# Kernel optimization log

Hardware: AMD Instinct MI355X
Metric: run time of the kernel (lower is better)

The kernel has to match this reference:

```python
import jax, jax.numpy as jnp
import numpy as np
import math

D_MODEL = 1024
N_HEADS = 16
D_K = D_MODEL // N_HEADS
B, S = 4, 2048
NEG_INF = -1e9


def setup_inputs() -> dict:
    key = jax.random.key(0)
    ks = jax.random.split(key, 12)
    scale = 1.0 / math.sqrt(D_MODEL)
    inp = {
        "q": jax.random.normal(ks[0], (B, S, D_MODEL), jnp.float32),
        "k": jax.random.normal(ks[1], (B, S, D_MODEL), jnp.float32),
        "v": jax.random.normal(ks[2], (B, S, D_MODEL), jnp.float32),
        "mask": jax.random.randint(ks[3], (1, 1, S, S), 0, 2, jnp.int32),
        "w_q": jax.random.normal(ks[4], (D_MODEL, D_MODEL), jnp.float32) * scale,
        "b_q": jnp.zeros((D_MODEL,), jnp.float32),
        "w_k": jax.random.normal(ks[5], (D_MODEL, D_MODEL), jnp.float32) * scale,
        "b_k": jnp.zeros((D_MODEL,), jnp.float32),
        "w_v": jax.random.normal(ks[6], (D_MODEL, D_MODEL), jnp.float32) * scale,
        "b_v": jnp.zeros((D_MODEL,), jnp.float32),
        "w_o": jax.random.normal(ks[7], (D_MODEL, D_MODEL), jnp.float32) * scale,
        "b_o": jnp.zeros((D_MODEL,), jnp.float32),
    }
    return inp


def reference(q, k, v, mask, w_q, b_q, w_k, b_k, w_v, b_v, w_o, b_o):
    # Linear projections (torch Linear: x @ W.T + b)
    query = q @ w_q.T + b_q
    key_p = k @ w_k.T + b_k
    value = v @ w_v.T + b_v
    # [B,S,D] -> [B,H,S,d_k]
    def split_heads(x):
        return x.reshape(B, S, N_HEADS, D_K).transpose(0, 2, 1, 3)
    qh, kh, vh = split_heads(query), split_heads(key_p), split_heads(value)
    # scores: [B,H,S,S]
    scores = jnp.einsum('bhqd,bhkd->bhqk', qh, kh) / math.sqrt(D_K)
    scores = jnp.where(mask == 0, NEG_INF, scores)
    probs = jax.nn.softmax(scores, axis=-1)
    # attention output: [B,H,S,d_k] -> [B,S,D]
    x = jnp.einsum('bhqk,bhkd->bhqd', probs, vh)
    x = x.transpose(0, 2, 1, 3).reshape(B, S, D_MODEL)
    return x @ w_o.T + b_o
```

## Files before the change

### kernel.cpp

```cpp
#include <hip/hip_runtime.h>


typedef __bf16  bf16x8 __attribute__((ext_vector_type(8)));
typedef float   f32x4  __attribute__((ext_vector_type(4)));
typedef float   f32x16 __attribute__((ext_vector_type(16)));
typedef float   fv4    __attribute__((ext_vector_type(4)));
typedef unsigned int uint;
typedef __attribute__((address_space(3))) char        as3c;
typedef __attribute__((address_space(1))) const char  as1c;

static __device__ __forceinline__ void gload16(const void* g, void* l) {
  __builtin_amdgcn_global_load_lds((as1c*)g, (as3c*)l, 16, 0, 0);
}
static __device__ __forceinline__ f32x4 mfma16(bf16x8 a, bf16x8 b, f32x4 c) {
  return __builtin_amdgcn_mfma_f32_16x16x32_bf16(a, b, c, 0, 0, 0);
}
static __device__ __forceinline__ f32x16 mfma32(bf16x8 a, bf16x8 b, f32x16 c) {
  return __builtin_amdgcn_mfma_f32_32x32x16_bf16(a, b, c, 0, 0, 0);
}
static __device__ __forceinline__ void st4bf(void* dst, float a, float b, float c, float d) {
  union { __bf16 h[4]; unsigned long long u; } x;
  x.h[0] = (__bf16)a; x.h[1] = (__bf16)b; x.h[2] = (__bf16)c; x.h[3] = (__bf16)d;
  *(unsigned long long*)dst = x.u;
}
static __device__ __forceinline__ uint pk2(float lo, float hi) {
  union { __bf16 h[2]; uint u; } x;
  x.h[0] = (__bf16)lo; x.h[1] = (__bf16)hi; return x.u;
}
static __device__ __forceinline__ f32x16 fconst16(float c) {
  f32x16 z;
#pragma unroll
  for (int i = 0; i < 16; ++i) z[i] = c;
  return z;
}

__global__ void cvt_w(const float* __restrict__ w0, const float* __restrict__ w1,
                      const float* __restrict__ w2, const float* __restrict__ w3,
                      __bf16* __restrict__ dst) {
  int i = (blockIdx.x * 256 + threadIdx.x) * 4;
  int seg = i >> 20, off = i & 1048575;
  const float* s = seg == 0 ? w0 : seg == 1 ? w1 : seg == 2 ? w2 : w3;
  fv4 v = *(const fv4*)(s + off);
  st4bf(dst + i, v[0], v[1], v[2], v[3]);
}

__global__ void pack_mask(const int* __restrict__ mask,
                          unsigned long long* __restrict__ out) {
  int wid = threadIdx.x >> 6, lane = threadIdx.x & 63;
  for (int w = blockIdx.x * 4 + wid; w < 2048 * 32; w += gridDim.x * 4) {
    int v = mask[(w >> 5) * 2048 + (w & 31) * 64 + lane];
    unsigned long long bits = __ballot(v != 0);
    if (lane == 0) out[w] = bits;
  }
}

template<int MODE>
__global__ __launch_bounds__(256, 3)
void gemm_bt(const void* __restrict__ Ap, const __bf16* __restrict__ Bw,
             const float* __restrict__ bias, void* __restrict__ Cp) {
  __shared__ __align__(16) char lds_a[2][8192];
  __shared__ __align__(16) char lds_b[2][8192];
  const int t = threadIdx.x;
  const int lane = t & 63, lr = lane & 15, lg = lane >> 4;
  const int wid = t >> 6, wr = wid >> 1, wc = wid & 1;
  const int bid = blockIdx.x;
  const int xcd = bid & 7, local = bid >> 3;
  const int rowStart = (xcd * 8 + (local >> 3)) * 128;
  const int colStart = (local & 7) * 128;

  const float*  Af = (const float*)Ap;
  const __bf16* Ah = (const __bf16*)Ap;
  fv4 ra[4];

  auto loadA = [&](int kt) {
    if constexpr (MODE < 3) {
#pragma unroll
      for (int rr = 0; rr < 4; ++rr) {
        int lin = rr * 1024 + t * 4;
        int row = lin >> 5, col = lin & 31;
        ra[rr] = *(const fv4*)(Af + (rowStart + row) * 1024 + kt + col);
      }
    }
  };
  auto writeA = [&](int buf) {
    if constexpr (MODE < 3) {
#pragma unroll
      for (int rr = 0; rr < 4; ++rr) {
        int lin = rr * 1024 + t * 4;
        st4bf(&lds_a[buf][lin * 2], ra[rr][0], ra[rr][1], ra[rr][2], ra[rr][3]);
      }
    }
  };
  auto stageB = [&](int buf, int kt) {
    if constexpr (MODE == 3) {
#pragma unroll
      for (int rr = 0; rr < 2; ++rr) {
        int lin = rr * 2048 + t * 8;
        int row = lin >> 5, col = lin & 31;
        gload16(Ah + (rowStart + row) * 1024 + kt + col, &lds_a[buf][lin * 2]);
      }
    }
#pragma unroll
    for (int rr = 0; rr < 2; ++rr) {
      int lin = rr * 2048 + t * 8;
      int row = lin >> 5, col = lin & 31;
      gload16(Bw + (colStart + row) * 1024 + kt + col, &lds_b[buf][lin * 2]);
    }
  };

  f32x4 acc[4][4];
#pragma unroll
  for (int m = 0; m < 4; ++m)
#pragma unroll
    for (int n = 0; n < 4; ++n) {
      acc[m][n][0] = 0.f; acc[m][n][1] = 0.f; acc[m][n][2] = 0.f; acc[m][n][3] = 0.f;
    }

  loadA(0); stageB(0, 0);
  int cur = 0;
  for (int it = 0; it < 32; ++it) {
    writeA(cur);
    __syncthreads();
    if (it + 1 < 32) { loadA((it + 1) * 32); stageB(cur ^ 1, (it + 1) * 32); }

    bf16x8 af[4], bfr[4];
#pragma unroll
    for (int m = 0; m < 4; ++m)
      af[m] = *(const bf16x8*)(&lds_a[cur][(wr * 64 + m * 16 + lr) * 64 + lg * 16]);
#pragma unroll
    for (int n = 0; n < 4; ++n)
      bfr[n] = *(const bf16x8*)(&lds_b[cur][(wc * 64 + n * 16 + lr) * 64 + lg * 16]);
#pragma unroll
    for (int m = 0; m < 4; ++m)
#pragma unroll
      for (int n = 0; n < 4; ++n)
        acc[m][n] = mfma16(af[m], bfr[n], acc[m][n]);
    cur ^= 1;
  }

#pragma unroll
  for (int n = 0; n < 4; ++n) {
    int col = colStart + wc * 64 + n * 16 + lr;
    float bv = bias[col];
#pragma unroll
    for (int m = 0; m < 4; ++m) {
      int rowb = rowStart + wr * 64 + m * 16 + lg * 4;
      if constexpr (MODE == 0 || MODE == 1) {
        __bf16* C = (__bf16*)Cp;
#pragma unroll
        for (int r = 0; r < 4; ++r) {
          float val = acc[m][n][r] + bv;
          if constexpr (MODE == 0) val *= 0.18033688011112042f;
          C[(rowb + r) * 1024 + col] = (__bf16)val;
        }
      } else if constexpr (MODE == 2) {
        __bf16* C = (__bf16*)Cp;
        int bb = rowb >> 11, s = rowb & 2047;
        st4bf(C + ((bb << 10) + col) * 2048 + s,
              acc[m][n][0] + bv, acc[m][n][1] + bv,
              acc[m][n][2] + bv, acc[m][n][3] + bv);
      } else {
        float* C = (float*)Cp;
#pragma unroll
        for (int r = 0; r < 4; ++r)
          C[(rowb + r) * 1024 + col] = acc[m][n][r] + bv;
      }
    }
  }
}

__global__ __launch_bounds__(256, 3)
void attn_fwd(const __bf16* __restrict__ Qp, const __bf16* __restrict__ Kp,
              const __bf16* __restrict__ Vt, const unsigned long long* __restrict__ Mb,
              __bf16* __restrict__ Xb) {
  __shared__ __align__(16) char lds[2][16384];
  const int t = threadIdx.x;
  const int lane = t & 63;
  const int l31 = lane & 31, hi = lane >> 5;
  const int wid = t >> 6;
  const int bid = blockIdx.x;
  const int nid = (bid & 7) * 128 + (bid >> 3);
  const int qblk = nid & 15, bh = nid >> 4;
  const int b = bh >> 4, h = bh & 15;
  const int q = qblk * 128 + wid * 32 + l31;

  bf16x8 qf[4];
#pragma unroll
  for (int c = 0; c < 4; ++c)
    qf[c] = *(const bf16x8*)(Qp + (b * 2048 + q) * 1024 + h * 64 + c * 16 + hi * 8);

  f32x16 xacc0 = fconst16(0.f), xacc1 = fconst16(0.f);
  float l_r = 0.f;

  auto stage = [&](int buf, int k0) {
#pragma unroll
    for (int rr = 0; rr < 2; ++rr) {
      int o = rr * 4096 + t * 16;
      int row = o >> 7, cb = o & 127;
      int cbs = cb ^ ((row & 7) << 4);
      gload16(Kp + (b * 2048 + k0 + row) * 1024 + h * 64 + (cbs >> 1), &lds[buf][o]);
      gload16(Vt + (bh * 64 + row) * 2048 + k0 + (cbs >> 1), &lds[buf][8192 + o]);
    }
  };

  stage(0, 0);
  int cur = 0;
  for (int it = 0; it < 32; ++it) {
    __syncthreads();
    if (it + 1 < 32) stage(cur ^ 1, (it + 1) * 64);

    const char* lk = lds[cur];
    const char* lv = lds[cur] + 8192;

    f32x16 sc0 = fconst16(-16.f), sc1 = fconst16(-16.f);
#pragma unroll
    for (int c = 0; c < 4; ++c) {
      {
        int krow = l31;
        int byo = (c * 32 + hi * 16) ^ ((krow & 7) << 4);
        bf16x8 kf = *(const bf16x8*)(lk + krow * 128 + byo);
        sc0 = mfma32(kf, qf[c], sc0);
      }
      {
        int krow = 32 + l31;
        int byo = (c * 32 + hi * 16) ^ ((krow & 7) << 4);
        bf16x8 kf = *(const bf16x8*)(lk + krow * 128 + byo);
        sc1 = mfma32(kf, qf[c], sc1);
      }
    }
    asm volatile("" : "+v"(sc0), "+v"(sc1));

    unsigned long long mw = Mb[q * 32 + it];
    uint mm0 = ((uint)mw) >> (4 * hi);
    uint mm1 = ((uint)(mw >> 32)) >> (4 * hi);
    float rs = 0.f;
#pragma unroll
    for (int r = 0; r < 16; ++r) {
      const int bit = (r & 3) + 8 * (r >> 2);
      float p0 = __builtin_amdgcn_exp2f(sc0[r]);
      float p1 = __builtin_amdgcn_exp2f(sc1[r]);
      uint z0 = (uint)((int)(mm0 << (31 - bit)) >> 31);
      uint z1 = (uint)((int)(mm1 << (31 - bit)) >> 31);
      p0 = __uint_as_float(__float_as_uint(p0) & z0);
      p1 = __uint_as_float(__float_as_uint(p1) & z1);
      sc0[r] = p0; sc1[r] = p1;
      rs += p0 + p1;
    }
    rs += __shfl_xor(rs, 32);
    l_r += rs;

    uint cp0[8], cp1[8];
#pragma unroll
    for (int m = 0; m < 8; ++m) {
      cp0[m] = pk2(sc0[2 * m], sc0[2 * m + 1]);
      cp1[m] = pk2(sc1[2 * m], sc1[2 * m + 1]);
    }

#define PV_SLICE(CPK, S) do {                                               \
      uint w0 = CPK[4 * ((S) & 1) + 0], w2 = CPK[4 * ((S) & 1) + 2];        \
      uint w1 = CPK[4 * ((S) & 1) + 1], w3 = CPK[4 * ((S) & 1) + 3];        \
      asm volatile("v_permlane32_swap_b32 %0, %1" : "+v"(w0), "+v"(w2));    \
      asm volatile("v_permlane32_swap_b32 %0, %1" : "+v"(w1), "+v"(w3));    \
      union { uint u[4]; bf16x8 v8; } pu;                                   \
      pu.u[0] = w0; pu.u[1] = w1; pu.u[2] = w2; pu.u[3] = w3;               \
      { int vrow = l31;                                                     \
        int byo = (((S) * 32 + hi * 16)) ^ ((vrow & 7) << 4);               \
        bf16x8 vf = *(const bf16x8*)(lv + vrow * 128 + byo);                \
        xacc0 = mfma32(vf, pu.v8, xacc0); }                                 \
      { int vrow = 32 + l31;                                                \
        int byo = (((S) * 32 + hi * 16)) ^ ((vrow & 7) << 4);               \
        bf16x8 vf = *(const bf16x8*)(lv + vrow * 128 + byo);                \
        xacc1 = mfma32(vf, pu.v8, xacc1); }                                 \
    } while (0)
    PV_SLICE(cp0, 0); PV_SLICE(cp0, 1); PV_SLICE(cp1, 2); PV_SLICE(cp1, 3);
#undef PV_SLICE
    cur ^= 1;
  }

  float inv = 1.f / l_r;
  __bf16* orow = Xb + (b * 2048 + q) * 1024 + h * 64 + 4 * hi;
#pragma unroll
  for (int g = 0; g < 4; ++g) {
    st4bf(orow + 8 * g,      xacc0[4 * g] * inv, xacc0[4 * g + 1] * inv,
                             xacc0[4 * g + 2] * inv, xacc0[4 * g + 3] * inv);
    st4bf(orow + 32 + 8 * g, xacc1[4 * g] * inv, xacc1[4 * g + 1] * inv,
                             xacc1[4 * g + 2] * inv, xacc1[4 * g + 3] * inv);
  }
}

extern "C" void kernel_launch(void* const* d_in, const int* in_sizes, int n_in,
                              void* d_out, int out_size, void* d_ws, size_t ws_size,
                              hipStream_t stream) {
  const float* q    = (const float*)d_in[0];
  const float* k    = (const float*)d_in[1];
  const float* v    = (const float*)d_in[2];
  const int*   mask = (const int*)d_in[3];
  const float* wq   = (const float*)d_in[4];
  const float* bq   = (const float*)d_in[5];
  const float* wk   = (const float*)d_in[6];
  const float* bk   = (const float*)d_in[7];
  const float* wv   = (const float*)d_in[8];
  const float* bv   = (const float*)d_in[9];
  const float* wo   = (const float*)d_in[10];
  const float* bo   = (const float*)d_in[11];

  char* ws = (char*)d_ws;
  __bf16* Wb  = (__bf16*)(ws);
  __bf16* Qp  = (__bf16*)(ws + (size_t)(8u  << 20));
  __bf16* Kp  = (__bf16*)(ws + (size_t)(24u << 20));
  __bf16* Vtb = (__bf16*)(ws + (size_t)(40u << 20));
  __bf16* Xb  = (__bf16*)(ws + (size_t)(56u << 20));
  unsigned long long* Mb = (unsigned long long*)(ws + (size_t)(72u << 20));

  cvt_w<<<4096, 256, 0, stream>>>(wq, wk, wv, wo, Wb);
  pack_mask<<<1024, 256, 0, stream>>>(mask, Mb);
  gemm_bt<0><<<512, 256, 0, stream>>>(q, Wb,              bq, Qp);
  gemm_bt<1><<<512, 256, 0, stream>>>(k, Wb + (1u << 20), bk, Kp);
  gemm_bt<2><<<512, 256, 0, stream>>>(v, Wb + (2u << 20), bv, Vtb);
  attn_fwd<<<1024, 256, 0, stream>>>(Qp, Kp, Vtb, Mb, Xb);
  gemm_bt<3><<<512, 256, 0, stream>>>(Xb, Wb + (3u << 20), bo, (float*)d_out);
}
```

Measured before the change: 419.0 us.

## Merge prep and QKV launches, compute softmax row sum via MFMA, add setprio

```diff
diff --git a/kernel.cpp b/kernel.cpp
--- a/kernel.cpp
+++ b/kernel.cpp
@@ -34,30 +34,132 @@
   return z;
 }
 
-__global__ void cvt_w(const float* __restrict__ w0, const float* __restrict__ w1,
-                      const float* __restrict__ w2, const float* __restrict__ w3,
-                      __bf16* __restrict__ dst) {
-  int i = (blockIdx.x * 256 + threadIdx.x) * 4;
-  int seg = i >> 20, off = i & 1048575;
-  const float* s = seg == 0 ? w0 : seg == 1 ? w1 : seg == 2 ? w2 : w3;
-  fv4 v = *(const fv4*)(s + off);
-  st4bf(dst + i, v[0], v[1], v[2], v[3]);
-}
-
-__global__ void pack_mask(const int* __restrict__ mask,
-                          unsigned long long* __restrict__ out) {
-  int wid = threadIdx.x >> 6, lane = threadIdx.x & 63;
-  for (int w = blockIdx.x * 4 + wid; w < 2048 * 32; w += gridDim.x * 4) {
-    int v = mask[(w >> 5) * 2048 + (w & 31) * 64 + lane];
-    unsigned long long bits = __ballot(v != 0);
-    if (lane == 0) out[w] = bits;
-  }
-}
-
-template<int MODE>
+__global__ void prep(const float* __restrict__ w0, const float* __restrict__ w1,
+                     const float* __restrict__ w2, const float* __restrict__ w3,
+                     __bf16* __restrict__ dst,
+                     const int* __restrict__ mask,
+                     unsigned long long* __restrict__ out) {
+  int bid = blockIdx.x;
+  if (bid < 4096) {
+    int i = (bid * 256 + threadIdx.x) * 4;
+    int seg = i >> 20, off = i & 1048575;
+    const float* s = seg == 0 ? w0 : seg == 1 ? w1 : seg == 2 ? w2 : w3;
+    fv4 v = *(const fv4*)(s + off);
+    st4bf(dst + i, v[0], v[1], v[2], v[3]);
+  } else {
+    int pb = bid - 4096;
+    int wid = threadIdx.x >> 6, lane = threadIdx.x & 63;
+    for (int w = pb * 4 + wid; w < 2048 * 32; w += 1024 * 4) {
+      int v = mask[(w >> 5) * 2048 + (w & 31) * 64 + lane];
+      unsigned long long bits = __ballot(v != 0);
+      if (lane == 0) out[w] = bits;
+    }
+  }
+}
+
 __global__ __launch_bounds__(256, 3)
-void gemm_bt(const void* __restrict__ Ap, const __bf16* __restrict__ Bw,
-             const float* __restrict__ bias, void* __restrict__ Cp) {
+void qkv_proj(const float* __restrict__ qin, const float* __restrict__ kin,
+              const float* __restrict__ vin, const __bf16* __restrict__ Wb,
+              const float* __restrict__ bq, const float* __restrict__ bk,
+              const float* __restrict__ bv,
+              __bf16* __restrict__ Qp, __bf16* __restrict__ Kp,
+              __bf16* __restrict__ Vt) {
+  __shared__ __align__(16) char lds_a[2][8192];
+  __shared__ __align__(16) char lds_b[2][8192];
+  const int t = threadIdx.x;
+  const int lane = t & 63, lr = lane & 15, lg = lane >> 4;
+  const int wid = t >> 6, wr = wid >> 1, wc = wid & 1;
+  const int x = blockIdx.x;
+  const int which = x >> 9, inner = x & 511;
+  const int xcd = inner & 7, local = inner >> 3;
+  const int rowStart = (xcd * 8 + (local >> 3)) * 128;
+  const int colStart = (local & 7) * 128;
+
+  const float*  A    = which == 0 ? qin : which == 1 ? kin : vin;
+  const __bf16* W    = Wb + (which << 20);
+  const float*  bias = which == 0 ? bq : which == 1 ? bk : bv;
+
+  fv4 ra[4];
+  auto loadA = [&](int kt) {
+#pragma unroll
+    for (int rr = 0; rr < 4; ++rr) {
+      int lin = rr * 1024 + t * 4;
+      int row = lin >> 5, col = lin & 31;
+      ra[rr] = *(const fv4*)(A + (rowStart + row) * 1024 + kt + col);
+    }
+  };
+  auto writeA = [&](int buf) {
+#pragma unroll
+    for (int rr = 0; rr < 4; ++rr) {
+      int lin = rr * 1024 + t * 4;
+      st4bf(&lds_a[buf][lin * 2], ra[rr][0], ra[rr][1], ra[rr][2], ra[rr][3]);
+    }
+  };
+  auto stageB = [&](int buf, int kt) {
+#pragma unroll
+    for (int rr = 0; rr < 2; ++rr) {
+      int lin = rr * 2048 + t * 8;
+      int row = lin >> 5, col = lin & 31;
+      gload16(W + (colStart + row) * 1024 + kt + col, &lds_b[buf][lin * 2]);
+    }
+  };
+
+  f32x4 acc[4][4];
+#pragma unroll
+  for (int m = 0; m < 4; ++m)
+#pragma unroll
+    for (int n = 0; n < 4; ++n) {
+      acc[m][n][0] = 0.f; acc[m][n][1] = 0.f; acc[m][n][2] = 0.f; acc[m][n][3] = 0.f;
+    }
+
+  loadA(0); stageB(0, 0);
+  int cur = 0;
+  for (int it = 0; it < 32; ++it) {
+    writeA(cur);
+    __syncthreads();
+    if (it + 1 < 32) { loadA((it + 1) * 32); stageB(cur ^ 1, (it + 1) * 32); }
+
+    bf16x8 af[4], bfr[4];
+#pragma unroll
+    for (int m = 0; m < 4; ++m)
+      af[m] = *(const bf16x8*)(&lds_a[cur][(wr * 64 + m * 16 + lr) * 64 + lg * 16]);
+#pragma unroll
+    for (int n = 0; n < 4; ++n)
+      bfr[n] = *(const bf16x8*)(&lds_b[cur][(wc * 64 + n * 16 + lr) * 64 + lg * 16]);
+#pragma unroll
+    for (int m = 0; m < 4; ++m)
+#pragma unroll
+      for (int n = 0; n < 4; ++n)
+        acc[m][n] = mfma16(af[m], bfr[n], acc[m][n]);
+    cur ^= 1;
+  }
+
+  const float scale = which == 0 ? 0.18033688011112042f : 1.0f;
+#pragma unroll
+  for (int n = 0; n < 4; ++n) {
+    int col = colStart + wc * 64 + n * 16 + lr;
+    float bvv = bias[col];
+#pragma unroll
+    for (int m = 0; m < 4; ++m) {
+      int rowb = rowStart + wr * 64 + m * 16 + lg * 4;
+      if (which == 2) {
+        int bb = rowb >> 11, s = rowb & 2047;
+        st4bf(Vt + ((bb << 10) + col) * 2048 + s,
+              acc[m][n][0] + bvv, acc[m][n][1] + bvv,
+              acc[m][n][2] + bvv, acc[m][n][3] + bvv);
+      } else {
+        __bf16* C = which == 0 ? Qp : Kp;
+#pragma unroll
+        for (int r = 0; r < 4; ++r)
+          C[(rowb + r) * 1024 + col] = (__bf16)((acc[m][n][r] + bvv) * scale);
+      }
+    }
+  }
+}
+
+__global__ __launch_bounds__(256, 3)
+void gemm_out(const __bf16* __restrict__ Ah, const __bf16* __restrict__ Bw,
+              const float* __restrict__ bias, float* __restrict__ Cp) {
   __shared__ __align__(16) char lds_a[2][8192];
   __shared__ __align__(16) char lds_b[2][8192];
   const int t = threadIdx.x;
@@ -68,42 +170,12 @@
   const int rowStart = (xcd * 8 + (local >> 3)) * 128;
   const int colStart = (local & 7) * 128;
 
-  const float*  Af = (const float*)Ap;
-  const __bf16* Ah = (const __bf16*)Ap;
-  fv4 ra[4];
-
-  auto loadA = [&](int kt) {
-    if constexpr (MODE < 3) {
-#pragma unroll
-      for (int rr = 0; rr < 4; ++rr) {
-        int lin = rr * 1024 + t * 4;
-        int row = lin >> 5, col = lin & 31;
-        ra[rr] = *(const fv4*)(Af + (rowStart + row) * 1024 + kt + col);
-      }
-    }
-  };
-  auto writeA = [&](int buf) {
-    if constexpr (MODE < 3) {
-#pragma unroll
-      for (int rr = 0; rr < 4; ++rr) {
-        int lin = rr * 1024 + t * 4;
-        st4bf(&lds_a[buf][lin * 2], ra[rr][0], ra[rr][1], ra[rr][2], ra[rr][3]);
-      }
-    }
-  };
-  auto stageB = [&](int buf, int kt) {
-    if constexpr (MODE == 3) {
-#pragma unroll
-      for (int rr = 0; rr < 2; ++rr) {
-        int lin = rr * 2048 + t * 8;
-        int row = lin >> 5, col = lin & 31;
-        gload16(Ah + (rowStart + row) * 1024 + kt + col, &lds_a[buf][lin * 2]);
-      }
-    }
+  auto stageAB = [&](int buf, int kt) {
 #pragma unroll
     for (int rr = 0; rr < 2; ++rr) {
       int lin = rr * 2048 + t * 8;
       int row = lin >> 5, col = lin & 31;
+      gload16(Ah + (rowStart + row) * 1024 + kt + col, &lds_a[buf][lin * 2]);
       gload16(Bw + (colStart + row) * 1024 + kt + col, &lds_b[buf][lin * 2]);
     }
   };
@@ -116,12 +188,11 @@
       acc[m][n][0] = 0.f; acc[m][n][1] = 0.f; acc[m][n][2] = 0.f; acc[m][n][3] = 0.f;
     }
 
-  loadA(0); stageB(0, 0);
+  stageAB(0, 0);
   int cur = 0;
   for (int it = 0; it < 32; ++it) {
-    writeA(cur);
     __syncthreads();
-    if (it + 1 < 32) { loadA((it + 1) * 32); stageB(cur ^ 1, (it + 1) * 32); }
+    if (it + 1 < 32) stageAB(cur ^ 1, (it + 1) * 32);
 
     bf16x8 af[4], bfr[4];
 #pragma unroll
@@ -141,30 +212,13 @@
 #pragma unroll
   for (int n = 0; n < 4; ++n) {
     int col = colStart + wc * 64 + n * 16 + lr;
-    float bv = bias[col];
+    float bvv = bias[col];
 #pragma unroll
     for (int m = 0; m < 4; ++m) {
       int rowb = rowStart + wr * 64 + m * 16 + lg * 4;
-      if constexpr (MODE == 0 || MODE == 1) {
-        __bf16* C = (__bf16*)Cp;
-#pragma unroll
-        for (int r = 0; r < 4; ++r) {
-          float val = acc[m][n][r] + bv;
-          if constexpr (MODE == 0) val *= 0.18033688011112042f;
-          C[(rowb + r) * 1024 + col] = (__bf16)val;
-        }
-      } else if constexpr (MODE == 2) {
-        __bf16* C = (__bf16*)Cp;
-        int bb = rowb >> 11, s = rowb & 2047;
-        st4bf(C + ((bb << 10) + col) * 2048 + s,
-              acc[m][n][0] + bv, acc[m][n][1] + bv,
-              acc[m][n][2] + bv, acc[m][n][3] + bv);
-      } else {
-        float* C = (float*)Cp;
-#pragma unroll
-        for (int r = 0; r < 4; ++r)
-          C[(rowb + r) * 1024 + col] = acc[m][n][r] + bv;
-      }
+#pragma unroll
+      for (int r = 0; r < 4; ++r)
+        Cp[(rowb + r) * 1024 + col] = acc[m][n][r] + bvv;
     }
   }
 }
@@ -189,8 +243,11 @@
   for (int c = 0; c < 4; ++c)
     qf[c] = *(const bf16x8*)(Qp + (b * 2048 + q) * 1024 + h * 64 + c * 16 + hi * 8);
 
+  union { uint u[4]; bf16x8 v8; } ones;
+  { uint o2 = pk2(1.f, 1.f); ones.u[0] = o2; ones.u[1] = o2; ones.u[2] = o2; ones.u[3] = o2; }
+
   f32x16 xacc0 = fconst16(0.f), xacc1 = fconst16(0.f);
-  float l_r = 0.f;
+  f32x16 lacc  = fconst16(0.f);
 
   auto stage = [&](int buf, int k0) {
 #pragma unroll
@@ -213,6 +270,7 @@
     const char* lv = lds[cur] + 8192;
 
     f32x16 sc0 = fconst16(-16.f), sc1 = fconst16(-16.f);
+    __builtin_amdgcn_s_setprio(1);
 #pragma unroll
     for (int c = 0; c < 4; ++c) {
       {
@@ -228,12 +286,12 @@
         sc1 = mfma32(kf, qf[c], sc1);
       }
     }
+    __builtin_amdgcn_s_setprio(0);
     asm volatile("" : "+v"(sc0), "+v"(sc1));
 
     unsigned long long mw = Mb[q * 32 + it];
     uint mm0 = ((uint)mw) >> (4 * hi);
     uint mm1 = ((uint)(mw >> 32)) >> (4 * hi);
-    float rs = 0.f;
 #pragma unroll
     for (int r = 0; r < 16; ++r) {
       const int bit = (r & 3) + 8 * (r >> 2);
@@ -241,13 +299,9 @@
       float p1 = __builtin_amdgcn_exp2f(sc1[r]);
       uint z0 = (uint)((int)(mm0 << (31 - bit)) >> 31);
       uint z1 = (uint)((int)(mm1 << (31 - bit)) >> 31);
-      p0 = __uint_as_float(__float_as_uint(p0) & z0);
-      p1 = __uint_as_float(__float_as_uint(p1) & z1);
-      sc0[r] = p0; sc1[r] = p1;
-      rs += p0 + p1;
-    }
-    rs += __shfl_xor(rs, 32);
-    l_r += rs;
+      sc0[r] = __uint_as_float(__float_as_uint(p0) & z0);
+      sc1[r] = __uint_as_float(__float_as_uint(p1) & z1);
+    }
 
     uint cp0[8], cp1[8];
 #pragma unroll
@@ -256,6 +310,7 @@
       cp1[m] = pk2(sc1[2 * m], sc1[2 * m + 1]);
     }
 
+    __builtin_amdgcn_s_setprio(1);
 #define PV_SLICE(CPK, S) do {                                               \
       uint w0 = CPK[4 * ((S) & 1) + 0], w2 = CPK[4 * ((S) & 1) + 2];        \
       uint w1 = CPK[4 * ((S) & 1) + 1], w3 = CPK[4 * ((S) & 1) + 3];        \
@@ -271,13 +326,15 @@
         int byo = (((S) * 32 + hi * 16)) ^ ((vrow & 7) << 4);               \
         bf16x8 vf = *(const bf16x8*)(lv + vrow * 128 + byo);                \
         xacc1 = mfma32(vf, pu.v8, xacc1); }                                 \
+      lacc = mfma32(ones.v8, pu.v8, lacc);                                  \
     } while (0)
     PV_SLICE(cp0, 0); PV_SLICE(cp0, 1); PV_SLICE(cp1, 2); PV_SLICE(cp1, 3);
 #undef PV_SLICE
+    __builtin_amdgcn_s_setprio(0);
     cur ^= 1;
   }
 
-  float inv = 1.f / l_r;
+  float inv = 1.f / lacc[0];
   __bf16* orow = Xb + (b * 2048 + q) * 1024 + h * 64 + 4 * hi;
 #pragma unroll
   for (int g = 0; g < 4; ++g) {
@@ -312,11 +369,8 @@
   __bf16* Xb  = (__bf16*)(ws + (size_t)(56u << 20));
   unsigned long long* Mb = (unsigned long long*)(ws + (size_t)(72u << 20));
 
-  cvt_w<<<4096, 256, 0, stream>>>(wq, wk, wv, wo, Wb);
-  pack_mask<<<1024, 256, 0, stream>>>(mask, Mb);
-  gemm_bt<0><<<512, 256, 0, stream>>>(q, Wb,              bq, Qp);
-  gemm_bt<1><<<512, 256, 0, stream>>>(k, Wb + (1u << 20), bk, Kp);
-  gemm_bt<2><<<512, 256, 0, stream>>>(v, Wb + (2u << 20), bv, Vtb);
+  prep<<<5120, 256, 0, stream>>>(wq, wk, wv, wo, Wb, mask, Mb);
+  qkv_proj<<<1536, 256, 0, stream>>>(q, k, v, Wb, bq, bk, bv, Qp, Kp, Vtb);
   attn_fwd<<<1024, 256, 0, stream>>>(Qp, Kp, Vtb, Mb, Xb);
-  gemm_bt<3><<<512, 256, 0, stream>>>(Xb, Wb + (3u << 20), bo, (float*)d_out);
-}
+  gemm_out<<<512, 256, 0, stream>>>(Xb, Wb + (3u << 20), bo, (float*)d_out);
+}
```

Result: no change. 414.6 us (-1.0%).
